# Kernel optimization log

Measured on AMD Instinct MI355X. Metric: run time of the kernel, lower is better.

## Reference

```python
import jax, jax.numpy as jnp
import numpy as np

EPS = 1e-8  # torch nn.CosineSimilarity default eps


def _cos(a, b):
    # cosine similarity along last axis with torch-style eps clamping
    dot = jnp.sum(a * b, axis=-1)
    na = jnp.maximum(jnp.linalg.norm(a, axis=-1), EPS)
    nb = jnp.maximum(jnp.linalg.norm(b, axis=-1), EPS)
    return dot / (na * nb)


def _segment_means(feat, idx):
    # feat: [B, T, D]; idx: [B, 2*S] interleaved (start, end) pairs, -1 sentinel.
    # Returns (means [B, S, D] zeroed where invalid, valid [B, S] bool).
    B, T, D = feat.shape
    starts = idx[:, 0::2]  # [B, S]
    ends = idx[:, 1::2]    # [B, S]
    # break at first start == -1 (cumulative validity, like the python `break`)
    valid = jnp.cumprod((starts >= 0).astype(jnp.int32), axis=1).astype(bool)
    # end == start means a single row at `start` (num == 0 branch)
    seg_len = jnp.maximum(ends - starts, 1)  # [B, S]
    t = jnp.arange(T)  # [T]
    in_seg = (t[None, None, :] >= starts[:, :, None]) & (
        t[None, None, :] < (starts + seg_len)[:, :, None]
    )
    mask = (in_seg & valid[:, :, None]).astype(feat.dtype)  # [B, S, T]
    seg_sum = jnp.einsum('bst,btd->bsd', mask, feat)
    means = seg_sum / seg_len[:, :, None].astype(feat.dtype)
    return means, valid


def reference(feat_x, index_pos, index_neg):
    # positive (cycle) segment means and center
    pos_means, pos_valid = _segment_means(feat_x, index_pos)  # [B,S,D], [B,S]
    pos_cnt = jnp.sum(pos_valid, axis=1).astype(feat_x.dtype)  # [B]
    center = jnp.sum(pos_means, axis=1) / pos_cnt[:, None]     # [B, D] (invalid already zero)

    cos_pos = _cos(pos_means, center[:, None, :])              # [B, S]
    loss1 = jnp.sum(jnp.where(pos_valid, 1.0 - cos_pos, 0.0), axis=1) / pos_cnt  # [B]

    # negative (non-cycle) segment means vs. center
    neg_means, neg_valid = _segment_means(feat_x, index_neg)
    neg_cnt = jnp.sum(neg_valid, axis=1).astype(feat_x.dtype)
    cos_neg = _cos(neg_means, center[:, None, :])              # [B, S]
    loss2_terms = jnp.exp(-(1.0 - cos_neg))
    loss2 = jnp.sum(jnp.where(neg_valid, loss2_terms, 0.0), axis=1) / neg_cnt  # [B]

    return jnp.mean(loss1 + loss2)


def setup_inputs() -> dict:
    key = jax.random.key(0)
    k1, k2, k3 = jax.random.split(key, 3)
    B, T, D, S2 = 64, 2048, 256, 32
    feat_x = jax.random.normal(k1, (B, T, D), dtype=jnp.float32)
    # sorted per-row ints -> every (start, end) pair satisfies start <= end
    index_pos = jnp.sort(jax.random.randint(k2, (B, S2), 0, T), axis=1)
    index_neg = jnp.sort(jax.random.randint(k3, (B, S2), 0, T), axis=1)
    return {"feat_x": feat_x, "index_pos": index_pos, "index_neg": index_neg}
```

## Files before the change

kernel.cpp:

```cpp
#include <hip/hip_runtime.h>
#include <math.h>

#define BB 64
#define TT 2048
#define DD 256
#define SS 16
#define CEPS 1e-8f

__global__ void seg_mean_kernel(const float* __restrict__ feat,
                                const int* __restrict__ idx_pos,
                                const int* __restrict__ idx_neg,
                                float* __restrict__ means,
                                int* __restrict__ validf) {
    int blk = blockIdx.x;
    int b   = blk >> 5;
    int ss  = blk & 31;
    int set = ss >> 4;
    int s   = ss & 15;
    const int* row = (set == 0 ? idx_pos : idx_neg) + b * 32;

    int v = 1;
    for (int j = 0; j <= s; ++j) v &= (row[2 * j] >= 0) ? 1 : 0;

    int start = row[2 * s];
    int end   = row[2 * s + 1];
    int seg_len = end - start;
    if (seg_len < 1) seg_len = 1;
    int t0 = start < 0 ? 0 : start;
    int t1 = start + seg_len;
    if (t1 > TT) t1 = TT;

    int tid = threadIdx.x;
    int d4  = tid & 63;
    int r   = tid >> 6;

    float4 acc = make_float4(0.f, 0.f, 0.f, 0.f);
    if (v) {
        const float4* fp = (const float4*)(feat + (size_t)b * TT * DD);
        for (int t = t0 + r; t < t1; t += 4) {
            float4 x = fp[(size_t)t * 64 + d4];
            acc.x += x.x; acc.y += x.y; acc.z += x.z; acc.w += x.w;
        }
    }

    __shared__ float4 red[256];
    red[tid] = acc;
    __syncthreads();
    if (r == 0) {
        float4 a0 = red[d4];
        float4 a1 = red[d4 + 64];
        float4 a2 = red[d4 + 128];
        float4 a3 = red[d4 + 192];
        float inv = 1.0f / (float)seg_len;
        float4 m;
        m.x = (a0.x + a1.x + a2.x + a3.x) * inv;
        m.y = (a0.y + a1.y + a2.y + a3.y) * inv;
        m.z = (a0.z + a1.z + a2.z + a3.z) * inv;
        m.w = (a0.w + a1.w + a2.w + a3.w) * inv;
        float4* mp = (float4*)(means + (((size_t)b * 2 + set) * SS + s) * DD);
        mp[d4] = m;
    }
    if (tid == 0) validf[(b * 2 + set) * SS + s] = v;
}

__device__ __forceinline__ float2 block_reduce2(float x, float y, float* sbuf) {
#pragma unroll
    for (int off = 32; off > 0; off >>= 1) {
        x += __shfl_down(x, off, 64);
        y += __shfl_down(y, off, 64);
    }
    int wave = threadIdx.x >> 6;
    int lane = threadIdx.x & 63;
    if (lane == 0) { sbuf[wave] = x; sbuf[4 + wave] = y; }
    __syncthreads();
    float rx = sbuf[0] + sbuf[1] + sbuf[2] + sbuf[3];
    float ry = sbuf[4] + sbuf[5] + sbuf[6] + sbuf[7];
    __syncthreads();
    return make_float2(rx, ry);
}

__global__ void loss_kernel(const float* __restrict__ means,
                            const int* __restrict__ validf,
                            float* __restrict__ loss_b) {
    __shared__ float sbuf[8];
    int b = blockIdx.x;
    int d = threadIdx.x;
    const float* pm = means + (size_t)b * 2 * SS * DD;
    const float* nm = pm + SS * DD;
    const int* pv = validf + b * 2 * SS;
    const int* nv = pv + SS;

    int pcnt = 0, ncnt = 0;
    for (int s = 0; s < SS; ++s) { pcnt += (pv[s] != 0); ncnt += (nv[s] != 0); }

    float c = 0.f;
#pragma unroll
    for (int s = 0; s < SS; ++s) c += pm[s * DD + d];
    float pc = (float)pcnt;
    c /= pc;

    float2 rc = block_reduce2(c * c, 0.f, sbuf);
    float nc = fmaxf(sqrtf(rc.x), CEPS);

    float loss1 = 0.f;
    for (int s = 0; s < SS; ++s) {
        float a = pm[s * DD + d];
        float2 r2 = block_reduce2(a * c, a * a, sbuf);
        float na = fmaxf(sqrtf(r2.y), CEPS);
        float cosv = r2.x / (na * nc);
        if (pv[s]) loss1 += 1.0f - cosv;
    }
    float loss2 = 0.f;
    for (int s = 0; s < SS; ++s) {
        float a = nm[s * DD + d];
        float2 r2 = block_reduce2(a * c, a * a, sbuf);
        float na = fmaxf(sqrtf(r2.y), CEPS);
        float cosv = r2.x / (na * nc);
        if (nv[s]) loss2 += expf(cosv - 1.0f);
    }
    if (d == 0) loss_b[b] = loss1 / pc + loss2 / (float)ncnt;
}

__global__ void final_kernel(const float* __restrict__ loss_b,
                             float* __restrict__ out) {
    float x = loss_b[threadIdx.x];
#pragma unroll
    for (int off = 32; off > 0; off >>= 1) x += __shfl_down(x, off, 64);
    if (threadIdx.x == 0) out[0] = x / (float)BB;
}

extern "C" void kernel_launch(void* const* d_in, const int* in_sizes, int n_in,
                              void* d_out, int out_size, void* d_ws, size_t ws_size,
                              hipStream_t stream) {
    const float* feat = (const float*)d_in[0];
    const int* ipos   = (const int*)d_in[1];
    const int* ineg   = (const int*)d_in[2];
    float* out = (float*)d_out;

    char* ws = (char*)d_ws;
    size_t means_bytes = (size_t)BB * 2 * SS * DD * sizeof(float);
    size_t valid_bytes = (size_t)BB * 2 * SS * sizeof(int);
    float* means  = (float*)ws;
    int*   validf = (int*)(ws + means_bytes);
    float* loss_b = (float*)(ws + means_bytes + valid_bytes);

    seg_mean_kernel<<<BB * 2 * SS, 256, 0, stream>>>(feat, ipos, ineg, means, validf);
    loss_kernel<<<BB, 256, 0, stream>>>(means, validf, loss_b);
    final_kernel<<<1, 64, 0, stream>>>(loss_b, out);
}
```

Measured before the change: 236.2 us.

## Unroll segment-sum loads, wave-parallel cosine loss, fuse final reduction via atomics

The segment-mean kernel now unrolls its row loop four ways with independent accumulators, so more loads are in flight per thread. The loss kernel gives each wave its own segments and reduces with wave shuffles, replacing 32 block-wide reductions that each needed two barriers. The final kernel is dropped: each block atomically adds its scaled loss into an output that is zeroed first by a memset. This makes the float summation order nondeterministic and adds a memset call to the launch sequence.

```diff
diff --git a/kernel.cpp b/kernel.cpp
--- a/kernel.cpp
+++ b/kernel.cpp
@@ -7,11 +7,12 @@
 #define SS 16
 #define CEPS 1e-8f
 
-__global__ void seg_mean_kernel(const float* __restrict__ feat,
-                                const int* __restrict__ idx_pos,
-                                const int* __restrict__ idx_neg,
-                                float* __restrict__ means,
-                                int* __restrict__ validf) {
+__global__ __launch_bounds__(256) void seg_mean_kernel(
+        const float* __restrict__ feat,
+        const int* __restrict__ idx_pos,
+        const int* __restrict__ idx_neg,
+        float* __restrict__ means,
+        int* __restrict__ validf) {
     int blk = blockIdx.x;
     int b   = blk >> 5;
     int ss  = blk & 31;
@@ -34,99 +35,117 @@
     int d4  = tid & 63;
     int r   = tid >> 6;
 
-    float4 acc = make_float4(0.f, 0.f, 0.f, 0.f);
+    float4 a0 = make_float4(0.f, 0.f, 0.f, 0.f);
+    float4 a1 = a0, a2 = a0, a3 = a0;
     if (v) {
         const float4* fp = (const float4*)(feat + (size_t)b * TT * DD);
-        for (int t = t0 + r; t < t1; t += 4) {
+        int t = t0 + r;
+        for (; t + 12 < t1; t += 16) {
+            float4 x0 = fp[(size_t)t * 64 + d4];
+            float4 x1 = fp[(size_t)(t + 4) * 64 + d4];
+            float4 x2 = fp[(size_t)(t + 8) * 64 + d4];
+            float4 x3 = fp[(size_t)(t + 12) * 64 + d4];
+            a0.x += x0.x; a0.y += x0.y; a0.z += x0.z; a0.w += x0.w;
+            a1.x += x1.x; a1.y += x1.y; a1.z += x1.z; a1.w += x1.w;
+            a2.x += x2.x; a2.y += x2.y; a2.z += x2.z; a2.w += x2.w;
+            a3.x += x3.x; a3.y += x3.y; a3.z += x3.z; a3.w += x3.w;
+        }
+        for (; t < t1; t += 4) {
             float4 x = fp[(size_t)t * 64 + d4];
-            acc.x += x.x; acc.y += x.y; acc.z += x.z; acc.w += x.w;
+            a0.x += x.x; a0.y += x.y; a0.z += x.z; a0.w += x.w;
         }
     }
+    float4 acc;
+    acc.x = (a0.x + a1.x) + (a2.x + a3.x);
+    acc.y = (a0.y + a1.y) + (a2.y + a3.y);
+    acc.z = (a0.z + a1.z) + (a2.z + a3.z);
+    acc.w = (a0.w + a1.w) + (a2.w + a3.w);
 
     __shared__ float4 red[256];
     red[tid] = acc;
     __syncthreads();
     if (r == 0) {
-        float4 a0 = red[d4];
-        float4 a1 = red[d4 + 64];
-        float4 a2 = red[d4 + 128];
-        float4 a3 = red[d4 + 192];
+        float4 b0 = red[d4];
+        float4 b1 = red[d4 + 64];
+        float4 b2 = red[d4 + 128];
+        float4 b3 = red[d4 + 192];
         float inv = 1.0f / (float)seg_len;
         float4 m;
-        m.x = (a0.x + a1.x + a2.x + a3.x) * inv;
-        m.y = (a0.y + a1.y + a2.y + a3.y) * inv;
-        m.z = (a0.z + a1.z + a2.z + a3.z) * inv;
-        m.w = (a0.w + a1.w + a2.w + a3.w) * inv;
+        m.x = ((b0.x + b1.x) + (b2.x + b3.x)) * inv;
+        m.y = ((b0.y + b1.y) + (b2.y + b3.y)) * inv;
+        m.z = ((b0.z + b1.z) + (b2.z + b3.z)) * inv;
+        m.w = ((b0.w + b1.w) + (b2.w + b3.w)) * inv;
         float4* mp = (float4*)(means + (((size_t)b * 2 + set) * SS + s) * DD);
         mp[d4] = m;
     }
     if (tid == 0) validf[(b * 2 + set) * SS + s] = v;
 }
 
-__device__ __forceinline__ float2 block_reduce2(float x, float y, float* sbuf) {
-#pragma unroll
-    for (int off = 32; off > 0; off >>= 1) {
-        x += __shfl_down(x, off, 64);
-        y += __shfl_down(y, off, 64);
-    }
-    int wave = threadIdx.x >> 6;
-    int lane = threadIdx.x & 63;
-    if (lane == 0) { sbuf[wave] = x; sbuf[4 + wave] = y; }
-    __syncthreads();
-    float rx = sbuf[0] + sbuf[1] + sbuf[2] + sbuf[3];
-    float ry = sbuf[4] + sbuf[5] + sbuf[6] + sbuf[7];
-    __syncthreads();
-    return make_float2(rx, ry);
-}
+__global__ __launch_bounds__(256) void loss_kernel(
+        const float* __restrict__ means,
+        const int* __restrict__ validf,
+        float* __restrict__ out) {
+    __shared__ float cs[DD];
+    __shared__ float wred[4];
+    __shared__ float wl1[4], wl2[4];
 
-__global__ void loss_kernel(const float* __restrict__ means,
-                            const int* __restrict__ validf,
-                            float* __restrict__ loss_b) {
-    __shared__ float sbuf[8];
     int b = blockIdx.x;
-    int d = threadIdx.x;
+    int tid = threadIdx.x;
+    int lane = tid & 63;
+    int wave = tid >> 6;
+
     const float* pm = means + (size_t)b * 2 * SS * DD;
-    const float* nm = pm + SS * DD;
     const int* pv = validf + b * 2 * SS;
-    const int* nv = pv + SS;
 
     int pcnt = 0, ncnt = 0;
-    for (int s = 0; s < SS; ++s) { pcnt += (pv[s] != 0); ncnt += (nv[s] != 0); }
+#pragma unroll
+    for (int s = 0; s < SS; ++s) { pcnt += (pv[s] != 0); ncnt += (pv[SS + s] != 0); }
+    float pc = (float)pcnt;
 
     float c = 0.f;
 #pragma unroll
-    for (int s = 0; s < SS; ++s) c += pm[s * DD + d];
-    float pc = (float)pcnt;
+    for (int s = 0; s < SS; ++s) c += pm[s * DD + tid];
     c /= pc;
+    cs[tid] = c;
 
-    float2 rc = block_reduce2(c * c, 0.f, sbuf);
-    float nc = fmaxf(sqrtf(rc.x), CEPS);
+    float cc = c * c;
+#pragma unroll
+    for (int off = 32; off > 0; off >>= 1) cc += __shfl_down(cc, off, 64);
+    if (lane == 0) wred[wave] = cc;
+    __syncthreads();
+    float ncen = fmaxf(sqrtf((wred[0] + wred[1]) + (wred[2] + wred[3])), CEPS);
 
-    float loss1 = 0.f;
-    for (int s = 0; s < SS; ++s) {
-        float a = pm[s * DD + d];
-        float2 r2 = block_reduce2(a * c, a * a, sbuf);
-        float na = fmaxf(sqrtf(r2.y), CEPS);
-        float cosv = r2.x / (na * nc);
-        if (pv[s]) loss1 += 1.0f - cosv;
+    float l1 = 0.f, l2 = 0.f;
+    for (int g = wave; g < 2 * SS; g += 4) {
+        const float* m = pm + g * DD;
+        float dot = 0.f, nn = 0.f;
+#pragma unroll
+        for (int k = 0; k < 4; ++k) {
+            int d = lane + 64 * k;
+            float a = m[d];
+            dot += a * cs[d];
+            nn  += a * a;
+        }
+#pragma unroll
+        for (int off = 32; off > 0; off >>= 1) {
+            dot += __shfl_down(dot, off, 64);
+            nn  += __shfl_down(nn, off, 64);
+        }
+        if (lane == 0) {
+            float na = fmaxf(sqrtf(nn), CEPS);
+            float cosv = dot / (na * ncen);
+            if (g < SS) { if (pv[g]) l1 += 1.0f - cosv; }
+            else        { if (pv[g]) l2 += expf(cosv - 1.0f); }
+        }
     }
-    float loss2 = 0.f;
-    for (int s = 0; s < SS; ++s) {
-        float a = nm[s * DD + d];
-        float2 r2 = block_reduce2(a * c, a * a, sbuf);
-        float na = fmaxf(sqrtf(r2.y), CEPS);
-        float cosv = r2.x / (na * nc);
-        if (nv[s]) loss2 += expf(cosv - 1.0f);
+    if (lane == 0) { wl1[wave] = l1; wl2[wave] = l2; }
+    __syncthreads();
+    if (tid == 0) {
+        float L1 = (wl1[0] + wl1[1]) + (wl1[2] + wl1[3]);
+        float L2 = (wl2[0] + wl2[1]) + (wl2[2] + wl2[3]);
+        float val = L1 / pc + L2 / (float)ncnt;
+        atomicAdd(out, val * (1.0f / (float)BB));
     }
-    if (d == 0) loss_b[b] = loss1 / pc + loss2 / (float)ncnt;
-}
-
-__global__ void final_kernel(const float* __restrict__ loss_b,
-                             float* __restrict__ out) {
-    float x = loss_b[threadIdx.x];
-#pragma unroll
-    for (int off = 32; off > 0; off >>= 1) x += __shfl_down(x, off, 64);
-    if (threadIdx.x == 0) out[0] = x / (float)BB;
 }
 
 extern "C" void kernel_launch(void* const* d_in, const int* in_sizes, int n_in,
@@ -139,12 +158,10 @@
 
     char* ws = (char*)d_ws;
     size_t means_bytes = (size_t)BB * 2 * SS * DD * sizeof(float);
-    size_t valid_bytes = (size_t)BB * 2 * SS * sizeof(int);
     float* means  = (float*)ws;
     int*   validf = (int*)(ws + means_bytes);
-    float* loss_b = (float*)(ws + means_bytes + valid_bytes);
 
+    hipMemsetAsync(out, 0, sizeof(float), stream);
     seg_mean_kernel<<<BB * 2 * SS, 256, 0, stream>>>(feat, ipos, ineg, means, validf);
-    loss_kernel<<<BB, 256, 0, stream>>>(means, validf, loss_b);
-    final_kernel<<<1, 64, 0, stream>>>(loss_b, out);
+    loss_kernel<<<BB, 256, 0, stream>>>(means, validf, out);
 }
```

Result: faster. 202.9 us (-14.1%).
